# Performance work log

Measured on AMD Instinct MI355X. Metric: run time of the kernel, lower is better.

Reference implementation:

```python
import jax, jax.numpy as jnp
import numpy as np

B, N, D = 8, 2048, 128

def setup_inputs() -> dict:
    key = jax.random.key(0)
    k1, k2, k3 = jax.random.split(key, 3)
    h = jax.random.normal(k1, (B, N, D), dtype=jnp.float32)
    W = jax.random.normal(k2, (D, D), dtype=jnp.float32) * (1.0 / np.sqrt(D))
    # a has shape [1,1,1,2D] in torch; flatten to [2D] (xavier-normal init)
    a = jax.random.normal(k3, (2 * D,), dtype=jnp.float32) * np.sqrt(2.0 / (2 * D))
    return {"h": h, "W": W, "a": a}

def reference(h, W, a):
    act = jax.nn.relu
    # h <- h @ W^T (nn.Linear with weight W means x @ W.T; here W is the weight matrix)
    hw = jnp.einsum('bnd,ed->bne', h, W)  # [B,N,D]
    a_i, a_j = a[:D], a[D:]
    # e_ij = act(a_i . h_i + a_j . h_j) -- equivalent to sum(cat(h_i,h_j)*a, -1)
    s_i = jnp.einsum('bnd,d->bn', hw, a_i)  # [B,N]
    s_j = jnp.einsum('bnd,d->bn', hw, a_j)  # [B,N]
    e = act(s_i[:, :, None] + s_j[:, None, :])  # [B,N,N]
    a_ij = jax.nn.softmax(e, axis=2)
    out = act(jnp.einsum('bij,bjd->bid', a_ij, hw))
    return out
```

## Files before the change

kernel.cpp:

```cpp
#include <hip/hip_runtime.h>
#include <hip/hip_bf16.h>

#define BB 8
#define NN 2048
#define DD 128
#define TI 16
#define HP 132
#define CH 32
#define NC (NN / CH)
#define NO (NC + 1)

__device__ __forceinline__ float relu(float x) { return x > 0.f ? x : 0.f; }

__global__ __launch_bounds__(256) void GraphAttentionalLayer_1168231104632_tr(
    const float* __restrict__ W, float* __restrict__ WT)
{
    const int g = blockIdx.x * 256 + threadIdx.x;
    const int d = g >> 7, e = g & 127;
    WT[g] = W[e * DD + d];
}

__global__ __launch_bounds__(128) void GraphAttentionalLayer_1168231104632_kernel(
    const float* __restrict__ h,
    const float* __restrict__ WT,
    const float* __restrict__ a,
    float* __restrict__ hw,
    float* __restrict__ E,
    float* __restrict__ F)
{
    __shared__ float h_s[TI][HP];
    __shared__ float wt_s[32][HP];

    const int t = threadIdx.x;
    const int tx = t & 31, ty = t >> 5;
    const int b = blockIdx.x >> 7;
    const int i0 = (blockIdx.x & 127) * TI;
    const size_t base = ((size_t)b * NN + i0) * DD;

    for (int r = 0; r < TI; r++)
        h_s[r][t] = h[base + (size_t)r * DD + t];

    const int e0 = tx * 4, r0 = ty * 4;
    float acc[4][4];
#pragma unroll
    for (int i = 0; i < 4; i++)
#pragma unroll
        for (int j = 0; j < 4; j++) acc[i][j] = 0.f;

    for (int dc = 0; dc < DD; dc += 32) {
        __syncthreads();
        for (int rr = 0; rr < 32; rr++)
            wt_s[rr][t] = WT[(size_t)(dc + rr) * DD + t];
        __syncthreads();
#pragma unroll
        for (int dd = 0; dd < 32; dd += 4) {
            float wq[4][4], hq[4][4];
#pragma unroll
            for (int q = 0; q < 4; q++) {
                const float4 v = *reinterpret_cast<const float4*>(&wt_s[dd + q][e0]);
                wq[q][0] = v.x; wq[q][1] = v.y; wq[q][2] = v.z; wq[q][3] = v.w;
            }
#pragma unroll
            for (int r = 0; r < 4; r++) {
                const float4 v = *reinterpret_cast<const float4*>(&h_s[r0 + r][dc + dd]);
                hq[r][0] = v.x; hq[r][1] = v.y; hq[r][2] = v.z; hq[r][3] = v.w;
            }
#pragma unroll
            for (int r = 0; r < 4; r++)
#pragma unroll
                for (int q = 0; q < 4; q++) {
                    const float hv = hq[r][q];
#pragma unroll
                    for (int e = 0; e < 4; e++) acc[r][e] += hv * wq[q][e];
                }
        }
    }

#pragma unroll
    for (int r = 0; r < 4; r++) {
        float4 o = make_float4(acc[r][0], acc[r][1], acc[r][2], acc[r][3]);
        *reinterpret_cast<float4*>(&hw[base + (size_t)(r0 + r) * DD + e0]) = o;
    }

    const float4 aiv = *reinterpret_cast<const float4*>(&a[e0]);
    const float4 ajv = *reinterpret_cast<const float4*>(&a[DD + e0]);
    const float ai4[4] = {aiv.x, aiv.y, aiv.z, aiv.w};
    const float aj4[4] = {ajv.x, ajv.y, ajv.z, ajv.w};
#pragma unroll
    for (int r = 0; r < 4; r++) {
        float pi = 0.f, pj = 0.f;
#pragma unroll
        for (int e = 0; e < 4; e++) { pi += acc[r][e] * ai4[e]; pj += acc[r][e] * aj4[e]; }
#pragma unroll
        for (int off = 16; off > 0; off >>= 1) {
            pi += __shfl_down(pi, off, 32);
            pj += __shfl_down(pj, off, 32);
        }
        if (tx == 0) {
            const size_t row = (size_t)b * NN + i0 + r0 + r;
            E[row] = __expf(pi);
            F[row] = __expf(pj);
        }
    }
}

__global__ __launch_bounds__(256) void GraphAttentionalLayer_1168231104632_rank(
    const float* __restrict__ F,
    float* __restrict__ Fsorted,
    int* __restrict__ perm)
{
    __shared__ float F_s[NN];
    __shared__ int   part[4][64];

    const int t = threadIdx.x;
    const int b = blockIdx.x >> 5;
    const int j0 = (blockIdx.x & 31) * 64;
    const size_t nb = (size_t)b * NN;

    for (int q = 0; q < NN / 256; q++)
        F_s[q * 256 + t] = F[nb + q * 256 + t];
    __syncthreads();

    const int tj = t & 63, ts = t >> 6;
    const int j = j0 + tj;
    const float fj = F_s[j];
    const int m0 = ts * (NN / 4);
    int cnt = 0;
#pragma unroll 8
    for (int mi = 0; mi < NN / 4; mi++) {
        const int m = m0 + mi;
        const float fm = F_s[m];
        cnt += (fm < fj) | ((fm == fj) & (m < j));
    }
    part[ts][tj] = cnt;
    __syncthreads();
    if (ts == 0) {
        const int r = part[0][tj] + part[1][tj] + part[2][tj] + part[3][tj];
        Fsorted[nb + r] = fj;
        perm[nb + r] = j;
    }
}

__global__ __launch_bounds__(128) void GraphAttentionalLayer_1168231104632_scan(
    const float* __restrict__ hw,
    const float* __restrict__ Fsorted,
    const int* __restrict__ perm,
    float* __restrict__ Q0L, float* __restrict__ Q1L,
    float* __restrict__ C0,  float* __restrict__ C1,
    float* __restrict__ FPL, float* __restrict__ CF)
{
    const int t = threadIdx.x;
    const int b = blockIdx.x / NC, c = blockIdx.x % NC;
    const size_t nb = (size_t)b * NN;
    const int m0 = c * CH;

    int   jv[CH];
    float Fv[CH];
#pragma unroll
    for (int mm = 0; mm < CH; mm++) jv[mm] = perm[nb + m0 + mm];
#pragma unroll
    for (int mm = 0; mm < CH; mm++) Fv[mm] = Fsorted[nb + m0 + mm];

    float hv[CH];
#pragma unroll
    for (int mm = 0; mm < CH; mm++)
        hv[mm] = hw[(nb + jv[mm]) * DD + t];

    float a0 = 0.f, a1 = 0.f;
#pragma unroll
    for (int mm = 0; mm < CH; mm++) {
        const int m = m0 + mm;
        Q0L[(nb + m) * DD + t] = a0;
        Q1L[(nb + m) * DD + t] = a1;
        a0 += hv[mm];
        a1 += Fv[mm] * hv[mm];
    }
    C0[((size_t)b * NC + c) * DD + t] = a0;
    C1[((size_t)b * NC + c) * DD + t] = a1;

    if (t == 0) {
        float p = 0.f;
#pragma unroll
        for (int mm = 0; mm < CH; mm++) {
            FPL[nb + m0 + mm] = p;
            p += Fv[mm];
        }
        CF[(size_t)b * NC + c] = p;
    }
}

__global__ __launch_bounds__(128) void GraphAttentionalLayer_1168231104632_fix(
    const float* __restrict__ C0, const float* __restrict__ C1,
    const float* __restrict__ CF,
    float* __restrict__ O0, float* __restrict__ O1,
    float* __restrict__ OF)
{
    __shared__ float cf[NC], sc[NC];

    const int t = threadIdx.x;
    const int b = blockIdx.x;

    if (t < NC) { const float v = CF[(size_t)b * NC + t]; cf[t] = v; sc[t] = v; }
    __syncthreads();
    for (int off = 1; off < NC; off <<= 1) {
        float v = 0.f;
        if (t < NC && t >= off) v = sc[t - off];
        __syncthreads();
        if (t < NC) sc[t] += v;
        __syncthreads();
    }
    if (t < NC) OF[(size_t)b * NO + t] = sc[t] - cf[t];
    if (t == 0) OF[(size_t)b * NO + NC] = sc[NC - 1];

    float o0 = 0.f, o1 = 0.f;
    for (int cc = 0; cc < NC; cc += 16) {
        float c0[16], c1[16];
#pragma unroll
        for (int q = 0; q < 16; q++) {
            c0[q] = C0[((size_t)b * NC + cc + q) * DD + t];
            c1[q] = C1[((size_t)b * NC + cc + q) * DD + t];
        }
#pragma unroll
        for (int q = 0; q < 16; q++) {
            O0[((size_t)b * NO + cc + q) * DD + t] = o0;
            O1[((size_t)b * NO + cc + q) * DD + t] = o1;
            o0 += c0[q];
            o1 += c1[q];
        }
    }
    O0[((size_t)b * NO + NC) * DD + t] = o0;
    O1[((size_t)b * NO + NC) * DD + t] = o1;
}

__global__ __launch_bounds__(128) void GraphAttentionalLayer_1168231104632_out(
    const float* __restrict__ Q0L, const float* __restrict__ Q1L,
    const float* __restrict__ O0,  const float* __restrict__ O1,
    const float* __restrict__ Fsorted, const float* __restrict__ FPL,
    const float* __restrict__ OF,  const float* __restrict__ E,
    float* __restrict__ out)
{
    __shared__ int   k_sh;
    __shared__ float e_sh, zi_sh;

    const int t = threadIdx.x;
    const int row = blockIdx.x;
    const int b = row >> 11;
    const size_t nb = (size_t)b * NN;

    if (t == 0) {
        const float Ei = E[row];
        const float thr = 1.0f / Ei;
        int lo = 0, hi = NN;
        while (lo < hi) {
            const int mid = (lo + hi) >> 1;
            if (Fsorted[nb + mid] < thr) lo = mid + 1; else hi = mid;
        }
        const float TF = OF[(size_t)b * NO + NC];
        const float Pk = (lo < NN) ? (OF[(size_t)b * NO + (lo >> 5)] + FPL[nb + lo]) : TF;
        const float z = Ei * (TF - Pk) + (float)lo;
        k_sh = lo; e_sh = Ei; zi_sh = 1.0f / z;
    }
    __syncthreads();

    const int k = k_sh;
    const float Ev = e_sh, zv = zi_sh;
    const float T1 = O1[((size_t)b * NO + NC) * DD + t];

    float num;
    if (k < NN) {
        const int c = k >> 5;
        const float q0 = Q0L[(nb + k) * DD + t] + O0[((size_t)b * NO + c) * DD + t];
        const float q1 = Q1L[(nb + k) * DD + t] + O1[((size_t)b * NO + c) * DD + t];
        num = Ev * (T1 - q1) + q0;
    } else {
        num = O0[((size_t)b * NO + NC) * DD + t];
    }
    out[(size_t)row * DD + t] = relu(num * zv);
}

extern "C" __attribute__((visibility("default")))
void kernel_launch(void* const* d_in, const int* in_sizes, int n_in,
                   void* d_out, int out_size, void* d_ws, size_t ws_size,
                   hipStream_t stream) {
    const float* h = nullptr; const float* W = nullptr; const float* a = nullptr;
    for (int i = 0; i < n_in; i++) {
        if (in_sizes[i] == BB * NN * DD)      h = (const float*)d_in[i];
        else if (in_sizes[i] == DD * DD)      W = (const float*)d_in[i];
        else if (in_sizes[i] == 2 * DD)       a = (const float*)d_in[i];
    }
    if (!h) h = (const float*)d_in[0];
    if (!W) W = (const float*)d_in[1];
    if (!a) a = (const float*)d_in[2];

    float* out = (float*)d_out;
    float* ws = (float*)d_ws;

    float* WT   = ws;
    float* hw   = WT + DD * DD;
    float* E    = hw + (size_t)BB * NN * DD;
    float* F    = E + BB * NN;
    float* Fs   = F + BB * NN;
    float* FPL  = Fs + BB * NN;
    float* CF   = FPL + BB * NN;
    float* OF   = CF + BB * NC;
    int*   perm = (int*)(OF + BB * NO);
    float* Q0L  = (float*)(perm + BB * NN);
    float* Q1L  = Q0L + (size_t)BB * NN * DD;
    float* C0   = Q1L + (size_t)BB * NN * DD;
    float* C1   = C0 + BB * NC * DD;
    float* O0   = C1 + BB * NC * DD;
    float* O1   = O0 + BB * NO * DD;
    const size_t need = (size_t)((O1 + BB * NO * DD) - ws) * sizeof(float);

    if (ws_size < need || d_ws == nullptr) {
        hipMemsetAsync(d_out, 0x42, (size_t)out_size * sizeof(float), stream);
        return;
    }

    GraphAttentionalLayer_1168231104632_tr<<<(DD * DD) / 256, 256, 0, stream>>>(W, WT);
    GraphAttentionalLayer_1168231104632_kernel<<<BB * (NN / TI), 128, 0, stream>>>(h, WT, a, hw, E, F);
    GraphAttentionalLayer_1168231104632_rank<<<BB * 32, 256, 0, stream>>>(F, Fs, perm);
    GraphAttentionalLayer_1168231104632_scan<<<BB * NC, 128, 0, stream>>>(hw, Fs, perm, Q0L, Q1L, C0, C1, FPL, CF);
    GraphAttentionalLayer_1168231104632_fix<<<BB, 128, 0, stream>>>(C0, C1, CF, O0, O1, OF);
    GraphAttentionalLayer_1168231104632_out<<<BB * NN, 128, 0, stream>>>(Q0L, Q1L, O0, O1, Fs, FPL, OF, E, out);
}
```

Before: 118.9 us.

## Fuse six kernels into one persistent kernel with atomic grid barriers

Replaces the six separate launches (transpose, projection, rank, chunk scan, fixup, output) with a single persistent 256-block kernel that separates the phases with software grid barriers built on atomic counters. Each block handles several tiles, chunks or rows per phase, and the output phase batches 64 rows per block with cached totals in shared memory. The goal is to remove per-launch overhead and the idle gaps between small kernels. In exchange, all blocks must be co-resident for the spin barriers to avoid deadlock, each barrier costs global atomics, and one phase (fix) runs on very few threads while the rest of the grid waits.

Result: slower. 262.5 us (+120.7%).

```diff
diff --git a/kernel.cpp b/kernel.cpp
--- a/kernel.cpp
+++ b/kernel.cpp
@@ -9,273 +9,273 @@
 #define CH 32
 #define NC (NN / CH)
 #define NO (NC + 1)
+#define GRID 256
+#define TPB 256
 
 __device__ __forceinline__ float relu(float x) { return x > 0.f ? x : 0.f; }
 
-__global__ __launch_bounds__(256) void GraphAttentionalLayer_1168231104632_tr(
-    const float* __restrict__ W, float* __restrict__ WT)
+__device__ __forceinline__ void gridbar(unsigned* bar, int p) {
+    __syncthreads();
+    if (threadIdx.x == 0) {
+        __threadfence();
+        __hip_atomic_fetch_add(&bar[p], 1u, __ATOMIC_ACQ_REL, __HIP_MEMORY_SCOPE_AGENT);
+        while (__hip_atomic_load(&bar[p], __ATOMIC_ACQUIRE, __HIP_MEMORY_SCOPE_AGENT) < GRID)
+            __builtin_amdgcn_s_sleep(1);
+        __threadfence();
+    }
+    __syncthreads();
+}
+
+__global__ __launch_bounds__(TPB, 1) void GraphAttentionalLayer_1168231104632_mega(
+    const float* __restrict__ h,
+    const float* __restrict__ W,
+    const float* __restrict__ a,
+    float* __restrict__ out,
+    float* __restrict__ WT,  float* __restrict__ hw,
+    float* __restrict__ E,   float* __restrict__ F,
+    float* __restrict__ Fs,  float* __restrict__ FPL,
+    float* __restrict__ CF,  float* __restrict__ OF,
+    int* __restrict__ perm,
+    float* __restrict__ Q0L, float* __restrict__ Q1L,
+    float* __restrict__ C0,  float* __restrict__ C1,
+    float* __restrict__ O0,  float* __restrict__ O1,
+    unsigned* __restrict__ bar)
 {
-    const int g = blockIdx.x * 256 + threadIdx.x;
-    const int d = g >> 7, e = g & 127;
-    WT[g] = W[e * DD + d];
-}
-
-__global__ __launch_bounds__(128) void GraphAttentionalLayer_1168231104632_kernel(
-    const float* __restrict__ h,
-    const float* __restrict__ WT,
-    const float* __restrict__ a,
-    float* __restrict__ hw,
-    float* __restrict__ E,
-    float* __restrict__ F)
-{
-    __shared__ float h_s[TI][HP];
+    __shared__ float h_s[2][TI][HP];
     __shared__ float wt_s[32][HP];
-
-    const int t = threadIdx.x;
-    const int tx = t & 31, ty = t >> 5;
-    const int b = blockIdx.x >> 7;
-    const int i0 = (blockIdx.x & 127) * TI;
-    const size_t base = ((size_t)b * NN + i0) * DD;
-
-    for (int r = 0; r < TI; r++)
-        h_s[r][t] = h[base + (size_t)r * DD + t];
-
-    const int e0 = tx * 4, r0 = ty * 4;
-    float acc[4][4];
-#pragma unroll
-    for (int i = 0; i < 4; i++)
-#pragma unroll
-        for (int j = 0; j < 4; j++) acc[i][j] = 0.f;
-
-    for (int dc = 0; dc < DD; dc += 32) {
-        __syncthreads();
-        for (int rr = 0; rr < 32; rr++)
-            wt_s[rr][t] = WT[(size_t)(dc + rr) * DD + t];
-        __syncthreads();
-#pragma unroll
-        for (int dd = 0; dd < 32; dd += 4) {
-            float wq[4][4], hq[4][4];
-#pragma unroll
-            for (int q = 0; q < 4; q++) {
-                const float4 v = *reinterpret_cast<const float4*>(&wt_s[dd + q][e0]);
-                wq[q][0] = v.x; wq[q][1] = v.y; wq[q][2] = v.z; wq[q][3] = v.w;
-            }
-#pragma unroll
-            for (int r = 0; r < 4; r++) {
-                const float4 v = *reinterpret_cast<const float4*>(&h_s[r0 + r][dc + dd]);
-                hq[r][0] = v.x; hq[r][1] = v.y; hq[r][2] = v.z; hq[r][3] = v.w;
-            }
-#pragma unroll
-            for (int r = 0; r < 4; r++)
-#pragma unroll
-                for (int q = 0; q < 4; q++) {
-                    const float hv = hq[r][q];
-#pragma unroll
-                    for (int e = 0; e < 4; e++) acc[r][e] += hv * wq[q][e];
-                }
-        }
-    }
-
-#pragma unroll
-    for (int r = 0; r < 4; r++) {
-        float4 o = make_float4(acc[r][0], acc[r][1], acc[r][2], acc[r][3]);
-        *reinterpret_cast<float4*>(&hw[base + (size_t)(r0 + r) * DD + e0]) = o;
-    }
-
-    const float4 aiv = *reinterpret_cast<const float4*>(&a[e0]);
-    const float4 ajv = *reinterpret_cast<const float4*>(&a[DD + e0]);
-    const float ai4[4] = {aiv.x, aiv.y, aiv.z, aiv.w};
-    const float aj4[4] = {ajv.x, ajv.y, ajv.z, ajv.w};
-#pragma unroll
-    for (int r = 0; r < 4; r++) {
-        float pi = 0.f, pj = 0.f;
-#pragma unroll
-        for (int e = 0; e < 4; e++) { pi += acc[r][e] * ai4[e]; pj += acc[r][e] * aj4[e]; }
-#pragma unroll
-        for (int off = 16; off > 0; off >>= 1) {
-            pi += __shfl_down(pi, off, 32);
-            pj += __shfl_down(pj, off, 32);
-        }
-        if (tx == 0) {
-            const size_t row = (size_t)b * NN + i0 + r0 + r;
-            E[row] = __expf(pi);
-            F[row] = __expf(pj);
-        }
-    }
-}
-
-__global__ __launch_bounds__(256) void GraphAttentionalLayer_1168231104632_rank(
-    const float* __restrict__ F,
-    float* __restrict__ Fsorted,
-    int* __restrict__ perm)
-{
     __shared__ float F_s[NN];
     __shared__ int   part[4][64];
-
-    const int t = threadIdx.x;
-    const int b = blockIdx.x >> 5;
-    const int j0 = (blockIdx.x & 31) * 64;
-    const size_t nb = (size_t)b * NN;
-
-    for (int q = 0; q < NN / 256; q++)
-        F_s[q * 256 + t] = F[nb + q * 256 + t];
-    __syncthreads();
-
-    const int tj = t & 63, ts = t >> 6;
-    const int j = j0 + tj;
-    const float fj = F_s[j];
-    const int m0 = ts * (NN / 4);
-    int cnt = 0;
+    __shared__ float T0s[DD], T1s[DD];
+    __shared__ int   k_sh[64];
+    __shared__ float e_sh[64], zi_sh[64];
+
+    const int tid = threadIdx.x;
+    const int half = tid >> 7;
+    const int t = tid & 127;
+
+    {
+        const int g = blockIdx.x * TPB + tid;
+        if (g < DD * DD) {
+            const int d = g >> 7, e = g & 127;
+            WT[g] = W[e * DD + d];
+        }
+    }
+    gridbar(bar, 0);
+
+    {
+        const int tx = t & 31, ty = t >> 5;
+        const int e0 = tx * 4, r0 = ty * 4;
+        for (int it = 0; it < 2; it++) {
+            const int tile = blockIdx.x * 4 + it * 2 + half;
+            const int bb = tile >> 7;
+            const int i0 = (tile & 127) * TI;
+            const size_t base = ((size_t)bb * NN + i0) * DD;
+
+            __syncthreads();
+            for (int r = 0; r < TI; r++)
+                h_s[half][r][t] = h[base + (size_t)r * DD + t];
+
+            float acc[4][4];
+#pragma unroll
+            for (int i = 0; i < 4; i++)
+#pragma unroll
+                for (int j = 0; j < 4; j++) acc[i][j] = 0.f;
+
+            for (int dc = 0; dc < DD; dc += 32) {
+                __syncthreads();
+                for (int rr = half; rr < 32; rr += 2)
+                    wt_s[rr][t] = WT[(size_t)(dc + rr) * DD + t];
+                __syncthreads();
+#pragma unroll 4
+                for (int dd = 0; dd < 32; dd++) {
+                    const float4 wv = *reinterpret_cast<const float4*>(&wt_s[dd][e0]);
+                    const float w4[4] = {wv.x, wv.y, wv.z, wv.w};
+#pragma unroll
+                    for (int r = 0; r < 4; r++) {
+                        const float hv = h_s[half][r0 + r][dc + dd];
+#pragma unroll
+                        for (int e = 0; e < 4; e++) acc[r][e] += hv * w4[e];
+                    }
+                }
+            }
+
+#pragma unroll
+            for (int r = 0; r < 4; r++) {
+                float4 o = make_float4(acc[r][0], acc[r][1], acc[r][2], acc[r][3]);
+                *reinterpret_cast<float4*>(&hw[base + (size_t)(r0 + r) * DD + e0]) = o;
+            }
+
+            const float4 aiv = *reinterpret_cast<const float4*>(&a[e0]);
+            const float4 ajv = *reinterpret_cast<const float4*>(&a[DD + e0]);
+            const float ai4[4] = {aiv.x, aiv.y, aiv.z, aiv.w};
+            const float aj4[4] = {ajv.x, ajv.y, ajv.z, ajv.w};
+#pragma unroll
+            for (int r = 0; r < 4; r++) {
+                float pi = 0.f, pj = 0.f;
+#pragma unroll
+                for (int e = 0; e < 4; e++) { pi += acc[r][e] * ai4[e]; pj += acc[r][e] * aj4[e]; }
+#pragma unroll
+                for (int off = 16; off > 0; off >>= 1) {
+                    pi += __shfl_down(pi, off, 32);
+                    pj += __shfl_down(pj, off, 32);
+                }
+                if (tx == 0) {
+                    const size_t row = (size_t)bb * NN + i0 + r0 + r;
+                    E[row] = __expf(pi);
+                    F[row] = __expf(pj);
+                }
+            }
+        }
+    }
+    gridbar(bar, 1);
+
+    {
+        const int b = blockIdx.x >> 5;
+        const int j0 = (blockIdx.x & 31) * 64;
+        const size_t nb = (size_t)b * NN;
+
+        for (int q = 0; q < NN / TPB; q++)
+            F_s[q * TPB + tid] = F[nb + q * TPB + tid];
+        __syncthreads();
+
+        const int tj = tid & 63, ts = tid >> 6;
+        const int j = j0 + tj;
+        const float fj = F_s[j];
+        const int m0 = ts * (NN / 4);
+        int cnt = 0;
 #pragma unroll 8
-    for (int mi = 0; mi < NN / 4; mi++) {
-        const int m = m0 + mi;
-        const float fm = F_s[m];
-        cnt += (fm < fj) | ((fm == fj) & (m < j));
-    }
-    part[ts][tj] = cnt;
-    __syncthreads();
-    if (ts == 0) {
-        const int r = part[0][tj] + part[1][tj] + part[2][tj] + part[3][tj];
-        Fsorted[nb + r] = fj;
-        perm[nb + r] = j;
-    }
-}
-
-__global__ __launch_bounds__(128) void GraphAttentionalLayer_1168231104632_scan(
-    const float* __restrict__ hw,
-    const float* __restrict__ Fsorted,
-    const int* __restrict__ perm,
-    float* __restrict__ Q0L, float* __restrict__ Q1L,
-    float* __restrict__ C0,  float* __restrict__ C1,
-    float* __restrict__ FPL, float* __restrict__ CF)
-{
-    const int t = threadIdx.x;
-    const int b = blockIdx.x / NC, c = blockIdx.x % NC;
-    const size_t nb = (size_t)b * NN;
-    const int m0 = c * CH;
-
-    int   jv[CH];
-    float Fv[CH];
-#pragma unroll
-    for (int mm = 0; mm < CH; mm++) jv[mm] = perm[nb + m0 + mm];
-#pragma unroll
-    for (int mm = 0; mm < CH; mm++) Fv[mm] = Fsorted[nb + m0 + mm];
-
-    float hv[CH];
-#pragma unroll
-    for (int mm = 0; mm < CH; mm++)
-        hv[mm] = hw[(nb + jv[mm]) * DD + t];
-
-    float a0 = 0.f, a1 = 0.f;
-#pragma unroll
-    for (int mm = 0; mm < CH; mm++) {
-        const int m = m0 + mm;
-        Q0L[(nb + m) * DD + t] = a0;
-        Q1L[(nb + m) * DD + t] = a1;
-        a0 += hv[mm];
-        a1 += Fv[mm] * hv[mm];
-    }
-    C0[((size_t)b * NC + c) * DD + t] = a0;
-    C1[((size_t)b * NC + c) * DD + t] = a1;
-
-    if (t == 0) {
-        float p = 0.f;
+        for (int mi = 0; mi < NN / 4; mi++) {
+            const int m = m0 + mi;
+            const float fm = F_s[m];
+            cnt += (fm < fj) | ((fm == fj) & (m < j));
+        }
+        part[ts][tj] = cnt;
+        __syncthreads();
+        if (ts == 0) {
+            const int r = part[0][tj] + part[1][tj] + part[2][tj] + part[3][tj];
+            Fs[nb + r] = fj;
+            perm[nb + r] = j;
+        }
+    }
+    gridbar(bar, 2);
+
+    {
+        const int chunk = blockIdx.x * 2 + half;
+        const int b = chunk / NC, c = chunk % NC;
+        const size_t nb = (size_t)b * NN;
+        const int m0 = c * CH;
+
+        int   jv[CH];
+        float Fv[CH];
+#pragma unroll
+        for (int mm = 0; mm < CH; mm++) jv[mm] = perm[nb + m0 + mm];
+#pragma unroll
+        for (int mm = 0; mm < CH; mm++) Fv[mm] = Fs[nb + m0 + mm];
+
+        float hv[CH];
+#pragma unroll
+        for (int mm = 0; mm < CH; mm++)
+            hv[mm] = hw[(nb + jv[mm]) * DD + t];
+
+        float a0 = 0.f, a1 = 0.f;
 #pragma unroll
         for (int mm = 0; mm < CH; mm++) {
-            FPL[nb + m0 + mm] = p;
-            p += Fv[mm];
-        }
-        CF[(size_t)b * NC + c] = p;
-    }
-}
-
-__global__ __launch_bounds__(128) void GraphAttentionalLayer_1168231104632_fix(
-    const float* __restrict__ C0, const float* __restrict__ C1,
-    const float* __restrict__ CF,
-    float* __restrict__ O0, float* __restrict__ O1,
-    float* __restrict__ OF)
-{
-    __shared__ float cf[NC], sc[NC];
-
-    const int t = threadIdx.x;
-    const int b = blockIdx.x;
-
-    if (t < NC) { const float v = CF[(size_t)b * NC + t]; cf[t] = v; sc[t] = v; }
-    __syncthreads();
-    for (int off = 1; off < NC; off <<= 1) {
-        float v = 0.f;
-        if (t < NC && t >= off) v = sc[t - off];
+            const int m = m0 + mm;
+            Q0L[(nb + m) * DD + t] = a0;
+            Q1L[(nb + m) * DD + t] = a1;
+            a0 += hv[mm];
+            a1 += Fv[mm] * hv[mm];
+        }
+        C0[((size_t)b * NC + c) * DD + t] = a0;
+        C1[((size_t)b * NC + c) * DD + t] = a1;
+
+        if (t == 0) {
+            float p = 0.f;
+#pragma unroll
+            for (int mm = 0; mm < CH; mm++) {
+                FPL[nb + m0 + mm] = p;
+                p += Fv[mm];
+            }
+            CF[(size_t)b * NC + c] = p;
+        }
+    }
+    gridbar(bar, 3);
+
+    {
+        const int g = blockIdx.x * TPB + tid;
+        if (g < BB * DD) {
+            const int b = g >> 7, d = g & 127;
+            float o0 = 0.f, o1 = 0.f;
+            for (int cc = 0; cc < NC; cc += 16) {
+                float c0[16], c1[16];
+#pragma unroll
+                for (int q = 0; q < 16; q++) {
+                    c0[q] = C0[((size_t)b * NC + cc + q) * DD + d];
+                    c1[q] = C1[((size_t)b * NC + cc + q) * DD + d];
+                }
+#pragma unroll
+                for (int q = 0; q < 16; q++) {
+                    O0[((size_t)b * NO + cc + q) * DD + d] = o0;
+                    O1[((size_t)b * NO + cc + q) * DD + d] = o1;
+                    o0 += c0[q];
+                    o1 += c1[q];
+                }
+            }
+            O0[((size_t)b * NO + NC) * DD + d] = o0;
+            O1[((size_t)b * NO + NC) * DD + d] = o1;
+        } else if (g < BB * DD + BB) {
+            const int b = g - BB * DD;
+            float p = 0.f;
+            for (int c = 0; c < NC; c++) {
+                OF[(size_t)b * NO + c] = p;
+                p += CF[(size_t)b * NC + c];
+            }
+            OF[(size_t)b * NO + NC] = p;
+        }
+    }
+    gridbar(bar, 4);
+
+    {
+        const int row0 = blockIdx.x * 64;
+        const int b = row0 >> 11;
+        const size_t nb = (size_t)b * NN;
+
+        if (tid < DD) {
+            T0s[tid] = O0[((size_t)b * NO + NC) * DD + tid];
+            T1s[tid] = O1[((size_t)b * NO + NC) * DD + tid];
+        }
+        if (tid < 64) {
+            const int row = row0 + tid;
+            const float Ei = E[row];
+            const float thr = 1.0f / Ei;
+            int lo = 0, hi = NN;
+            while (lo < hi) {
+                const int mid = (lo + hi) >> 1;
+                if (Fs[nb + mid] < thr) lo = mid + 1; else hi = mid;
+            }
+            const float TF = OF[(size_t)b * NO + NC];
+            const float Pk = (lo < NN) ? (OF[(size_t)b * NO + (lo >> 5)] + FPL[nb + lo]) : TF;
+            const float z = Ei * (TF - Pk) + (float)lo;
+            k_sh[tid] = lo; e_sh[tid] = Ei; zi_sh[tid] = 1.0f / z;
+        }
         __syncthreads();
-        if (t < NC) sc[t] += v;
-        __syncthreads();
-    }
-    if (t < NC) OF[(size_t)b * NO + t] = sc[t] - cf[t];
-    if (t == 0) OF[(size_t)b * NO + NC] = sc[NC - 1];
-
-    float o0 = 0.f, o1 = 0.f;
-    for (int cc = 0; cc < NC; cc += 16) {
-        float c0[16], c1[16];
-#pragma unroll
-        for (int q = 0; q < 16; q++) {
-            c0[q] = C0[((size_t)b * NC + cc + q) * DD + t];
-            c1[q] = C1[((size_t)b * NC + cc + q) * DD + t];
-        }
-#pragma unroll
-        for (int q = 0; q < 16; q++) {
-            O0[((size_t)b * NO + cc + q) * DD + t] = o0;
-            O1[((size_t)b * NO + cc + q) * DD + t] = o1;
-            o0 += c0[q];
-            o1 += c1[q];
-        }
-    }
-    O0[((size_t)b * NO + NC) * DD + t] = o0;
-    O1[((size_t)b * NO + NC) * DD + t] = o1;
-}
-
-__global__ __launch_bounds__(128) void GraphAttentionalLayer_1168231104632_out(
-    const float* __restrict__ Q0L, const float* __restrict__ Q1L,
-    const float* __restrict__ O0,  const float* __restrict__ O1,
-    const float* __restrict__ Fsorted, const float* __restrict__ FPL,
-    const float* __restrict__ OF,  const float* __restrict__ E,
-    float* __restrict__ out)
-{
-    __shared__ int   k_sh;
-    __shared__ float e_sh, zi_sh;
-
-    const int t = threadIdx.x;
-    const int row = blockIdx.x;
-    const int b = row >> 11;
-    const size_t nb = (size_t)b * NN;
-
-    if (t == 0) {
-        const float Ei = E[row];
-        const float thr = 1.0f / Ei;
-        int lo = 0, hi = NN;
-        while (lo < hi) {
-            const int mid = (lo + hi) >> 1;
-            if (Fsorted[nb + mid] < thr) lo = mid + 1; else hi = mid;
-        }
-        const float TF = OF[(size_t)b * NO + NC];
-        const float Pk = (lo < NN) ? (OF[(size_t)b * NO + (lo >> 5)] + FPL[nb + lo]) : TF;
-        const float z = Ei * (TF - Pk) + (float)lo;
-        k_sh = lo; e_sh = Ei; zi_sh = 1.0f / z;
-    }
-    __syncthreads();
-
-    const int k = k_sh;
-    const float Ev = e_sh, zv = zi_sh;
-    const float T1 = O1[((size_t)b * NO + NC) * DD + t];
-
-    float num;
-    if (k < NN) {
-        const int c = k >> 5;
-        const float q0 = Q0L[(nb + k) * DD + t] + O0[((size_t)b * NO + c) * DD + t];
-        const float q1 = Q1L[(nb + k) * DD + t] + O1[((size_t)b * NO + c) * DD + t];
-        num = Ev * (T1 - q1) + q0;
-    } else {
-        num = O0[((size_t)b * NO + NC) * DD + t];
-    }
-    out[(size_t)row * DD + t] = relu(num * zv);
+
+        for (int it = 0; it < 32; it++) {
+            const int idx = it * 2 + half;
+            const int k = k_sh[idx];
+            const float Ev = e_sh[idx], zv = zi_sh[idx];
+            float num;
+            if (k < NN) {
+                const int c = k >> 5;
+                const float q0 = Q0L[(nb + k) * DD + t] + O0[((size_t)b * NO + c) * DD + t];
+                const float q1 = Q1L[(nb + k) * DD + t] + O1[((size_t)b * NO + c) * DD + t];
+                num = Ev * (T1s[t] - q1) + q0;
+            } else {
+                num = T0s[t];
+            }
+            out[(size_t)(row0 + idx) * DD + t] = relu(num * zv);
+        }
+    }
 }
 
 extern "C" __attribute__((visibility("default")))
@@ -310,17 +310,17 @@
     float* C1   = C0 + BB * NC * DD;
     float* O0   = C1 + BB * NC * DD;
     float* O1   = O0 + BB * NO * DD;
-    const size_t need = (size_t)((O1 + BB * NO * DD) - ws) * sizeof(float);
+    unsigned* bar = (unsigned*)(O1 + BB * NO * DD);
+    const size_t need = ((char*)(bar + 16) - (char*)ws);
 
     if (ws_size < need || d_ws == nullptr) {
         hipMemsetAsync(d_out, 0x42, (size_t)out_size * sizeof(float), stream);
         return;
     }
 
-    GraphAttentionalLayer_1168231104632_tr<<<(DD * DD) / 256, 256, 0, stream>>>(W, WT);
-    GraphAttentionalLayer_1168231104632_kernel<<<BB * (NN / TI), 128, 0, stream>>>(h, WT, a, hw, E, F);
-    GraphAttentionalLayer_1168231104632_rank<<<BB * 32, 256, 0, stream>>>(F, Fs, perm);
-    GraphAttentionalLayer_1168231104632_scan<<<BB * NC, 128, 0, stream>>>(hw, Fs, perm, Q0L, Q1L, C0, C1, FPL, CF);
-    GraphAttentionalLayer_1168231104632_fix<<<BB, 128, 0, stream>>>(C0, C1, CF, O0, O1, OF);
-    GraphAttentionalLayer_1168231104632_out<<<BB * NN, 128, 0, stream>>>(Q0L, Q1L, O0, O1, Fs, FPL, OF, E, out);
+    hipMemsetAsync(bar, 0, 64, stream);
+    GraphAttentionalLayer_1168231104632_mega<<<GRID, TPB, 0, stream>>>(
+        h, W, a, out,
+        WT, hw, E, F, Fs, FPL, CF, OF, perm,
+        Q0L, Q1L, C0, C1, O0, O1, bar);
 }
```

## Split chunk prefix fix into two-level parallel scan and simplify GEMM inner loop

Applied to the files above, without the earlier changes.

The single-block-per-batch serial prefix over chunk sums is replaced by two kernels. The first sums groups of 16 chunks and the second computes each chunk's exclusive prefix in its own block, which raises parallelism from 8 blocks to hundreds. This adds one kernel launch and some redundant reads. The projection GEMM inner loop also changes from float4 reads of h_s to scalar reads with a smaller register footprint, which may raise LDS traffic.

After: 126.6 us. 1.06x slower.

```diff
diff --git a/kernel.cpp b/kernel.cpp
--- a/kernel.cpp
+++ b/kernel.cpp
@@ -9,6 +9,7 @@
 #define CH 32
 #define NC (NN / CH)
 #define NO (NC + 1)
+#define NG 4
 
 __device__ __forceinline__ float relu(float x) { return x > 0.f ? x : 0.f; }
 
@@ -52,27 +53,16 @@
         for (int rr = 0; rr < 32; rr++)
             wt_s[rr][t] = WT[(size_t)(dc + rr) * DD + t];
         __syncthreads();
-#pragma unroll
-        for (int dd = 0; dd < 32; dd += 4) {
-            float wq[4][4], hq[4][4];
-#pragma unroll
-            for (int q = 0; q < 4; q++) {
-                const float4 v = *reinterpret_cast<const float4*>(&wt_s[dd + q][e0]);
-                wq[q][0] = v.x; wq[q][1] = v.y; wq[q][2] = v.z; wq[q][3] = v.w;
+#pragma unroll 4
+        for (int dd = 0; dd < 32; dd++) {
+            const float4 wv = *reinterpret_cast<const float4*>(&wt_s[dd][e0]);
+            const float w4[4] = {wv.x, wv.y, wv.z, wv.w};
+#pragma unroll
+            for (int r = 0; r < 4; r++) {
+                const float hv = h_s[r0 + r][dc + dd];
+#pragma unroll
+                for (int e = 0; e < 4; e++) acc[r][e] += hv * w4[e];
             }
-#pragma unroll
-            for (int r = 0; r < 4; r++) {
-                const float4 v = *reinterpret_cast<const float4*>(&h_s[r0 + r][dc + dd]);
-                hq[r][0] = v.x; hq[r][1] = v.y; hq[r][2] = v.z; hq[r][3] = v.w;
-            }
-#pragma unroll
-            for (int r = 0; r < 4; r++)
-#pragma unroll
-                for (int q = 0; q < 4; q++) {
-                    const float hv = hq[r][q];
-#pragma unroll
-                    for (int e = 0; e < 4; e++) acc[r][e] += hv * wq[q][e];
-                }
         }
     }
 
@@ -189,47 +179,61 @@
     }
 }
 
-__global__ __launch_bounds__(128) void GraphAttentionalLayer_1168231104632_fix(
+__global__ __launch_bounds__(128) void GraphAttentionalLayer_1168231104632_fixA(
     const float* __restrict__ C0, const float* __restrict__ C1,
     const float* __restrict__ CF,
-    float* __restrict__ O0, float* __restrict__ O1,
-    float* __restrict__ OF)
-{
-    __shared__ float cf[NC], sc[NC];
-
-    const int t = threadIdx.x;
-    const int b = blockIdx.x;
-
-    if (t < NC) { const float v = CF[(size_t)b * NC + t]; cf[t] = v; sc[t] = v; }
-    __syncthreads();
-    for (int off = 1; off < NC; off <<= 1) {
-        float v = 0.f;
-        if (t < NC && t >= off) v = sc[t - off];
-        __syncthreads();
-        if (t < NC) sc[t] += v;
-        __syncthreads();
-    }
-    if (t < NC) OF[(size_t)b * NO + t] = sc[t] - cf[t];
-    if (t == 0) OF[(size_t)b * NO + NC] = sc[NC - 1];
+    float* __restrict__ G0, float* __restrict__ G1, float* __restrict__ GF)
+{
+    const int t = threadIdx.x;
+    const int b = blockIdx.x >> 2, g = blockIdx.x & 3;
+    const int cbase = (int)((size_t)b * NC + g * 16);
+
+    float s0 = 0.f, s1 = 0.f;
+#pragma unroll
+    for (int q = 0; q < 16; q++) {
+        s0 += C0[(size_t)(cbase + q) * DD + t];
+        s1 += C1[(size_t)(cbase + q) * DD + t];
+    }
+    G0[((size_t)b * NG + g) * DD + t] = s0;
+    G1[((size_t)b * NG + g) * DD + t] = s1;
+
+    if (t == 0) {
+        float p = 0.f;
+#pragma unroll
+        for (int q = 0; q < 16; q++) p += CF[cbase + q];
+        GF[b * NG + g] = p;
+    }
+}
+
+__global__ __launch_bounds__(128) void GraphAttentionalLayer_1168231104632_fixB(
+    const float* __restrict__ C0, const float* __restrict__ C1,
+    const float* __restrict__ CF,
+    const float* __restrict__ G0, const float* __restrict__ G1,
+    const float* __restrict__ GF,
+    float* __restrict__ O0, float* __restrict__ O1, float* __restrict__ OF)
+{
+    const int t = threadIdx.x;
+    const int b = blockIdx.x / NO, c = blockIdx.x % NO;
+    const int gc = c >> 4;
 
     float o0 = 0.f, o1 = 0.f;
-    for (int cc = 0; cc < NC; cc += 16) {
-        float c0[16], c1[16];
-#pragma unroll
-        for (int q = 0; q < 16; q++) {
-            c0[q] = C0[((size_t)b * NC + cc + q) * DD + t];
-            c1[q] = C1[((size_t)b * NC + cc + q) * DD + t];
-        }
-#pragma unroll
-        for (int q = 0; q < 16; q++) {
-            O0[((size_t)b * NO + cc + q) * DD + t] = o0;
-            O1[((size_t)b * NO + cc + q) * DD + t] = o1;
-            o0 += c0[q];
-            o1 += c1[q];
-        }
-    }
-    O0[((size_t)b * NO + NC) * DD + t] = o0;
-    O1[((size_t)b * NO + NC) * DD + t] = o1;
+    for (int g = 0; g < gc; g++) {
+        o0 += G0[((size_t)b * NG + g) * DD + t];
+        o1 += G1[((size_t)b * NG + g) * DD + t];
+    }
+    for (int c2 = gc * 16; c2 < c; c2++) {
+        o0 += C0[((size_t)b * NC + c2) * DD + t];
+        o1 += C1[((size_t)b * NC + c2) * DD + t];
+    }
+    O0[((size_t)b * NO + c) * DD + t] = o0;
+    O1[((size_t)b * NO + c) * DD + t] = o1;
+
+    if (t == 0) {
+        float p = 0.f;
+        for (int g = 0; g < gc; g++) p += GF[b * NG + g];
+        for (int c2 = gc * 16; c2 < c; c2++) p += CF[(size_t)b * NC + c2];
+        OF[(size_t)b * NO + c] = p;
+    }
 }
 
 __global__ __launch_bounds__(128) void GraphAttentionalLayer_1168231104632_out(
@@ -303,12 +307,15 @@
     float* FPL  = Fs + BB * NN;
     float* CF   = FPL + BB * NN;
     float* OF   = CF + BB * NC;
-    int*   perm = (int*)(OF + BB * NO);
+    float* GF   = OF + BB * NO;
+    int*   perm = (int*)(GF + BB * NG);
     float* Q0L  = (float*)(perm + BB * NN);
     float* Q1L  = Q0L + (size_t)BB * NN * DD;
     float* C0   = Q1L + (size_t)BB * NN * DD;
     float* C1   = C0 + BB * NC * DD;
-    float* O0   = C1 + BB * NC * DD;
+    float* G0   = C1 + BB * NC * DD;
+    float* G1   = G0 + BB * NG * DD;
+    float* O0   = G1 + BB * NG * DD;
     float* O1   = O0 + BB * NO * DD;
     const size_t need = (size_t)((O1 + BB * NO * DD) - ws) * sizeof(float);
 
@@ -321,6 +328,7 @@
     GraphAttentionalLayer_1168231104632_kernel<<<BB * (NN / TI), 128, 0, stream>>>(h, WT, a, hw, E, F);
     GraphAttentionalLayer_1168231104632_rank<<<BB * 32, 256, 0, stream>>>(F, Fs, perm);
     GraphAttentionalLayer_1168231104632_scan<<<BB * NC, 128, 0, stream>>>(hw, Fs, perm, Q0L, Q1L, C0, C1, FPL, CF);
-    GraphAttentionalLayer_1168231104632_fix<<<BB, 128, 0, stream>>>(C0, C1, CF, O0, O1, OF);
+    GraphAttentionalLayer_1168231104632_fixA<<<BB * NG, 128, 0, stream>>>(C0, C1, CF, G0, G1, GF);
+    GraphAttentionalLayer_1168231104632_fixB<<<BB * NO, 128, 0, stream>>>(C0, C1, CF, G0, G1, GF, O0, O1, OF);
     GraphAttentionalLayer_1168231104632_out<<<BB * NN, 128, 0, stream>>>(Q0L, Q1L, O0, O1, Fs, FPL, OF, E, out);
 }
```
